# Performance work log

Hardware: AMD Instinct MI355X
Metric: run time of the kernel (lower is better)

The kernel has to match this reference:

```python
import jax, jax.numpy as jnp
import numpy as np

B, N, K0, SHARED = 32768, 64, 8, 2
DELTA = 1e-6
LOG100 = float(np.log(100.0))
LOG1MD = float(np.log(1.0 - DELTA))

def _log(t):
    # torch: log(x) = torch.log(x*100.0) - np.log(100.0)
    return jnp.log(t * 100.0) - LOG100

def _softplus(t):
    return jax.nn.softplus(t) + 0.001

def _logsigmoid(t):
    return -_softplus(-t)

def setup_inputs() -> dict:
    key = jax.random.key(0)
    k1, k2, k3 = jax.random.split(key, 3)
    return {
        "x": jax.random.normal(k1, (B, N), dtype=jnp.float32),
        "logdet": jnp.zeros((B, N), dtype=jnp.float32),
        "dsparams": jax.random.normal(k2, (B, N, 3, K0), dtype=jnp.float32),
        "shared_params": 0.1 * jax.random.normal(k3, (1, N, 3, SHARED), dtype=jnp.float32),
    }

def reference(x, logdet, dsparams, shared_params):
    Bx = x.shape[0]
    shared = jnp.broadcast_to(shared_params, (Bx,) + shared_params.shape[1:])
    dsp = jnp.concatenate([dsparams, shared], axis=-1)  # (B, N, 3, K)
    a = _softplus(dsp[:, :, 0])      # (B, N, K)
    b = dsp[:, :, 1]                  # (B, N, K)
    w_logits = dsp[:, :, 2]           # (B, N, K)
    w = jax.nn.softmax(w_logits, axis=2)
    pre_sigm = a * x[..., None] + b   # (B, N, K)
    x_pre = jnp.sum(w * jax.nn.sigmoid(pre_sigm), axis=2)  # (B, N)
    x_pre_clipped = x_pre * (1.0 - DELTA) + DELTA * 0.5
    xnew = _log(x_pre_clipped) - _log(1.0 - x_pre_clipped)
    logj = (jax.nn.log_softmax(w_logits, axis=2)
            + _logsigmoid(pre_sigm)
            + _logsigmoid(-pre_sigm)
            + _log(a))
    logj = jax.scipy.special.logsumexp(logj, axis=2)  # (B, N)
    logdet_out = logdet + logj + LOG1MD - (_log(x_pre_clipped) + _log(1.0 - x_pre_clipped))
    return xnew, logdet_out
```

## Files before the change

kernel.cpp:

```cpp
#include <hip/hip_runtime.h>
#include <math.h>

#define Bdim   32768
#define Ndim   64
#define K0dim  8
#define KSH    2
#define KT     10
#define BN     (Bdim * Ndim)
#define DELTA  1e-06f
#define LOG1MD (-1.0000005000001665e-06f)

__device__ __forceinline__ float log1pexp(float t) {
    float e = __expf(-fabsf(t));
    return fmaxf(t, 0.0f) + __logf(1.0f + e);
}

__global__ __launch_bounds__(256) void sigmoid_flow_kernel(
    const float* __restrict__ x,
    const float* __restrict__ logdet,
    const float* __restrict__ dsp,
    const float* __restrict__ shp,
    float* __restrict__ out)
{
    __shared__ float s_sh[Ndim * 6];
    for (int t = threadIdx.x; t < Ndim * 6; t += blockDim.x) s_sh[t] = shp[t];
    __syncthreads();

    int idx = blockIdx.x * blockDim.x + threadIdx.x;
    float xv = x[idx];
    float ld = logdet[idx];
    int n = idx & (Ndim - 1);

    const float4* p = (const float4*)(dsp + (size_t)idx * 24);
    float4 r0 = p[0], r1 = p[1];
    float4 r2 = p[2], r3 = p[3];
    float4 r4 = p[4], r5 = p[5];

    float ap[KT], bp[KT], wl[KT];
    ap[0]=r0.x; ap[1]=r0.y; ap[2]=r0.z; ap[3]=r0.w;
    ap[4]=r1.x; ap[5]=r1.y; ap[6]=r1.z; ap[7]=r1.w;
    bp[0]=r2.x; bp[1]=r2.y; bp[2]=r2.z; bp[3]=r2.w;
    bp[4]=r3.x; bp[5]=r3.y; bp[6]=r3.z; bp[7]=r3.w;
    wl[0]=r4.x; wl[1]=r4.y; wl[2]=r4.z; wl[3]=r4.w;
    wl[4]=r5.x; wl[5]=r5.y; wl[6]=r5.z; wl[7]=r5.w;

    const float* sh = &s_sh[n * 6];
    ap[8] = sh[0]; ap[9] = sh[1];
    bp[8] = sh[2]; bp[9] = sh[3];
    wl[8] = sh[4]; wl[9] = sh[5];

    float wmax = wl[0];
    #pragma unroll
    for (int k = 1; k < KT; ++k) wmax = fmaxf(wmax, wl[k]);
    float wexp[KT];
    float wsum = 0.0f;
    #pragma unroll
    for (int k = 0; k < KT; ++k) { wexp[k] = __expf(wl[k] - wmax); wsum += wexp[k]; }
    float inv_wsum = __fdividef(1.0f, wsum);
    float lwsum = __logf(wsum);

    float x_pre = 0.0f;
    float lj[KT];
    float ljmax = -3.0e38f;
    #pragma unroll
    for (int k = 0; k < KT; ++k) {
        float a   = log1pexp(ap[k]) + 0.001f;
        float pre = fmaf(a, xv, bp[k]);
        float e    = __expf(-fabsf(pre));
        float l1pe = __logf(1.0f + e);
        float sig  = ((pre >= 0.0f) ? 1.0f : e) * __fdividef(1.0f, 1.0f + e);
        x_pre += wexp[k] * sig;
        float lss = -(fabsf(pre) + 2.0f * l1pe) - 0.002f;
        float v = wl[k] + lss + __logf(a);
        lj[k] = v;
        ljmax = fmaxf(ljmax, v);
    }
    x_pre *= inv_wsum;

    float es = 0.0f;
    #pragma unroll
    for (int k = 0; k < KT; ++k) es += __expf(lj[k] - ljmax);
    float lse = ljmax + __logf(es) - wmax - lwsum;

    float xc   = x_pre * (1.0f - DELTA) + DELTA * 0.5f;
    float lxc  = __logf(xc);
    float l1xc = __logf(1.0f - xc);

    out[idx]      = lxc - l1xc;
    out[BN + idx] = ld + lse + LOG1MD - (lxc + l1xc);
}

extern "C" void kernel_launch(void* const* d_in, const int* in_sizes, int n_in,
                              void* d_out, int out_size, void* d_ws, size_t ws_size,
                              hipStream_t stream) {
    const float* x   = (const float*)d_in[0];
    const float* ld  = (const float*)d_in[1];
    const float* dsp = (const float*)d_in[2];
    const float* shp = (const float*)d_in[3];
    float* out = (float*)d_out;

    const int block = 256;
    const int grid  = BN / block;
    sigmoid_flow_kernel<<<grid, block, 0, stream>>>(x, ld, dsp, shp, out);
}
```

Measured before the change: 292.3 us.

## Stage dsparams through LDS with coalesced loads and simplify logsumexp algebra

The per-point dsparams rows are loaded as coalesced float4 reads across the block into a padded shared-memory tile (stride 25), replacing strided per-thread 96-byte loads. The log-Jacobian logsumexp is rewritten as the log of a weighted sum of a*sigmoid*(1-sigmoid), which removes the max pass, the per-k log calls and the second exp pass. The softmax max subtraction is also dropped, so large weight logits could overflow exp. The kernel adds 25KB of LDS per block, which may limit occupancy.

```diff
diff --git a/kernel.cpp b/kernel.cpp
--- a/kernel.cpp
+++ b/kernel.cpp
@@ -3,17 +3,13 @@
 
 #define Bdim   32768
 #define Ndim   64
-#define K0dim  8
-#define KSH    2
 #define KT     10
 #define BN     (Bdim * Ndim)
 #define DELTA  1e-06f
 #define LOG1MD (-1.0000005000001665e-06f)
 
-__device__ __forceinline__ float log1pexp(float t) {
-    float e = __expf(-fabsf(t));
-    return fmaxf(t, 0.0f) + __logf(1.0f + e);
-}
+#define PTS    256
+#define LSTR   25
 
 __global__ __launch_bounds__(256) void sigmoid_flow_kernel(
     const float* __restrict__ x,
@@ -22,69 +18,65 @@
     const float* __restrict__ shp,
     float* __restrict__ out)
 {
+    __shared__ float s[PTS * LSTR];
     __shared__ float s_sh[Ndim * 6];
-    for (int t = threadIdx.x; t < Ndim * 6; t += blockDim.x) s_sh[t] = shp[t];
+
+    const int t = threadIdx.x;
+
+    for (int i = t; i < Ndim * 6; i += PTS) s_sh[i] = shp[i];
+
+    const float4* g = (const float4*)dsp + (size_t)blockIdx.x * (PTS * 6);
+    #pragma unroll
+    for (int j = 0; j < 6; ++j) {
+        int q = t + PTS * j;
+        float4 v = g[q];
+        int f  = q * 4;
+        int pt = f / 24;
+        int pm = f - pt * 24;
+        float* d = &s[pt * LSTR + pm];
+        d[0] = v.x; d[1] = v.y; d[2] = v.z; d[3] = v.w;
+    }
     __syncthreads();
 
-    int idx = blockIdx.x * blockDim.x + threadIdx.x;
-    float xv = x[idx];
-    float ld = logdet[idx];
-    int n = idx & (Ndim - 1);
+    const int idx = blockIdx.x * PTS + t;
+    const float xv = x[idx];
+    const float ld = logdet[idx];
 
-    const float4* p = (const float4*)(dsp + (size_t)idx * 24);
-    float4 r0 = p[0], r1 = p[1];
-    float4 r2 = p[2], r3 = p[3];
-    float4 r4 = p[4], r5 = p[5];
+    const float* m  = &s[t * LSTR];
+    const float* sh = &s_sh[(t & 63) * 6];
 
     float ap[KT], bp[KT], wl[KT];
-    ap[0]=r0.x; ap[1]=r0.y; ap[2]=r0.z; ap[3]=r0.w;
-    ap[4]=r1.x; ap[5]=r1.y; ap[6]=r1.z; ap[7]=r1.w;
-    bp[0]=r2.x; bp[1]=r2.y; bp[2]=r2.z; bp[3]=r2.w;
-    bp[4]=r3.x; bp[5]=r3.y; bp[6]=r3.z; bp[7]=r3.w;
-    wl[0]=r4.x; wl[1]=r4.y; wl[2]=r4.z; wl[3]=r4.w;
-    wl[4]=r5.x; wl[5]=r5.y; wl[6]=r5.z; wl[7]=r5.w;
-
-    const float* sh = &s_sh[n * 6];
+    #pragma unroll
+    for (int k = 0; k < 8; ++k) {
+        ap[k] = m[k]; bp[k] = m[8 + k]; wl[k] = m[16 + k];
+    }
     ap[8] = sh[0]; ap[9] = sh[1];
     bp[8] = sh[2]; bp[9] = sh[3];
     wl[8] = sh[4]; wl[9] = sh[5];
 
-    float wmax = wl[0];
-    #pragma unroll
-    for (int k = 1; k < KT; ++k) wmax = fmaxf(wmax, wl[k]);
-    float wexp[KT];
-    float wsum = 0.0f;
-    #pragma unroll
-    for (int k = 0; k < KT; ++k) { wexp[k] = __expf(wl[k] - wmax); wsum += wexp[k]; }
-    float inv_wsum = __fdividef(1.0f, wsum);
-    float lwsum = __logf(wsum);
-
-    float x_pre = 0.0f;
-    float lj[KT];
-    float ljmax = -3.0e38f;
+    float wsum = 0.0f, x_pre = 0.0f, S = 0.0f;
     #pragma unroll
     for (int k = 0; k < KT; ++k) {
-        float a   = log1pexp(ap[k]) + 0.001f;
+        float we = __expf(wl[k]);
+        wsum += we;
+        float t0 = ap[k];
+        float e1 = __expf(-fabsf(t0));
+        float a  = fmaxf(t0, 0.0f) + __logf(1.0f + e1) + 0.001f;
         float pre = fmaf(a, xv, bp[k]);
-        float e    = __expf(-fabsf(pre));
-        float l1pe = __logf(1.0f + e);
-        float sig  = ((pre >= 0.0f) ? 1.0f : e) * __fdividef(1.0f, 1.0f + e);
-        x_pre += wexp[k] * sig;
-        float lss = -(fabsf(pre) + 2.0f * l1pe) - 0.002f;
-        float v = wl[k] + lss + __logf(a);
-        lj[k] = v;
-        ljmax = fmaxf(ljmax, v);
+        float e  = __expf(-fabsf(pre));
+        float r  = __builtin_amdgcn_rcpf(1.0f + e);
+        float sig = ((pre >= 0.0f) ? 1.0f : e) * r;
+        x_pre = fmaf(we, sig, x_pre);
+        S = fmaf(we * a, (e * r) * r, S);
     }
-    x_pre *= inv_wsum;
+    float invw = __builtin_amdgcn_rcpf(wsum);
+    x_pre *= invw;
+    float lse = __logf(S * invw) - 0.002f;
 
-    float es = 0.0f;
-    #pragma unroll
-    for (int k = 0; k < KT; ++k) es += __expf(lj[k] - ljmax);
-    float lse = ljmax + __logf(es) - wmax - lwsum;
-
-    float xc   = x_pre * (1.0f - DELTA) + DELTA * 0.5f;
+    float xc   = fmaf(x_pre, 1.0f - DELTA, 0.5f * DELTA);
+    float omxc = fmaf(-(1.0f - DELTA), x_pre, 1.0f - 0.5f * DELTA);
     float lxc  = __logf(xc);
-    float l1xc = __logf(1.0f - xc);
+    float l1xc = __logf(omxc);
 
     out[idx]      = lxc - l1xc;
     out[BN + idx] = ld + lse + LOG1MD - (lxc + l1xc);
@@ -99,7 +91,6 @@
     const float* shp = (const float*)d_in[3];
     float* out = (float*)d_out;
 
-    const int block = 256;
-    const int grid  = BN / block;
-    sigmoid_flow_kernel<<<grid, block, 0, stream>>>(x, ld, dsp, shp, out);
+    const int grid = BN / PTS;
+    sigmoid_flow_kernel<<<grid, PTS, 0, stream>>>(x, ld, dsp, shp, out);
 }
```

Result: no change. 291.3 us (-0.3%).
